# Kernel optimization log

Measured on AMD Instinct MI355X. Metric: run time of the kernel, lower is better.

## Reference

```python
import jax, jax.numpy as jnp
import numpy as np

FIRST_USER_FEATURE = 64
TOP_K = 10
SIG_TAU = 1.0
TAU_NDCG = 0.1
TAU_DIV = 0.1
EPS = 1e-10
SINKHORN_ITERS = 5


def sinkhorn_scaling(mat):
    # Fixed 5 iterations (torch version has a data-dependent early break with
    # tol=1e-6 that essentially never triggers at these temperatures).
    for _ in range(SINKHORN_ITERS):
        mat = mat / jnp.clip(mat.sum(axis=1, keepdims=True), EPS)
        mat = mat / jnp.clip(mat.sum(axis=2, keepdims=True), EPS)
    return mat


def calc_p_sort(score, tau):
    # NeuralSort-style soft permutation. score: (U, N) -> p: (U, N, N)
    s = score.astype(jnp.float32)
    N = s.shape[-1]
    # A_k = sum_j |s_k - s_j|  (matches a_s.sum(dim=-1) in torch; symmetric)
    a_sum = jnp.abs(s[:, :, None] - s[:, None, :]).sum(axis=-1)  # (U, N)
    v = (N + 1 - 2 * jnp.arange(1, N + 1)).astype(jnp.float32)   # (N,)
    logits = v[None, :, None] * s[:, None, :] - a_sum[:, None, :]  # (U, N, N)
    p = jax.nn.softmax(logits / tau, axis=-1)
    return sinkhorn_scaling(p)


def calc_dcg(rel):
    # rel: (U, N); take first TOP_K positions, log2 discount
    r = rel[:, :TOP_K]
    disc = jnp.log2(jnp.arange(2, TOP_K + 2, dtype=jnp.float32))
    return ((2.0 ** r - 1.0) / disc).sum(axis=1)


def calc_ndcg(p_sort, score, rel):
    approx_rel = jnp.einsum('uij,uj->ui', p_sort, rel.astype(jnp.float32))
    approx_dcg = calc_dcg(approx_rel)
    idx = jnp.argsort(-score, axis=1)  # descending sort indices
    rel_by_model = jnp.take_along_axis(rel, idx, axis=1)
    dcg = calc_dcg(rel_by_model)
    best_dcg = calc_dcg(-jnp.sort(-rel, axis=1))
    return approx_dcg / best_dcg, dcg / best_dcg


def dissimilarity_metric(items):
    # 1 - pairwise cosine similarity between item feature vectors. items: (U,N,F)
    n = items / jnp.clip(jnp.linalg.norm(items, axis=-1, keepdims=True), 1e-8)
    return 1.0 - jnp.einsum('uif,ujf->uij', n, n)


def calc_diversity(batch, score, p_sort):
    items = batch[:, :, :FIRST_USER_FEATURE]
    N = batch.shape[1]
    w = jnp.arange(N, 0, -1, dtype=jnp.float32)                  # row weights N..1
    approx_rank = jnp.einsum('uij,i->uj', p_sort, w)             # (U, N)
    approx_rank = jax.nn.sigmoid(SIG_TAU * (approx_rank - (N - TOP_K)))
    # zero_below_diagonal == keep strictly-upper triangle
    approx_mat = jnp.triu(approx_rank[:, :, None] * approx_rank[:, None, :], k=1)
    # real rank: rank 1 = lowest score, rank N = highest (argsort of argsort)
    real_rank = (jnp.argsort(jnp.argsort(score, axis=1), axis=1) + 1).astype(jnp.float32)
    real_rank = jnp.clip(real_rank - (N - TOP_K), 0.0, 1.0)
    real_mat = jnp.triu(real_rank[:, :, None] * real_rank[:, None, :], k=1)
    dis = jnp.triu(dissimilarity_metric(items), k=1)
    approx_div = (approx_mat * dis).sum(axis=(1, 2)) / jax.lax.stop_gradient(approx_mat.sum(axis=(1, 2)))
    div = (real_mat * dis).sum(axis=(1, 2)) / real_mat.sum(axis=(1, 2))
    return approx_div, div


def setup_inputs() -> dict:
    key = jax.random.key(0)
    k1, k2, k3, k4 = jax.random.split(key, 4)
    U, N, F = 128, 512, 80
    return {
        'batch': jax.random.normal(k1, (U, N, F), dtype=jnp.float32),
        'model_score_for_div': jax.random.normal(k2, (U, N), dtype=jnp.float32),
        'model_score_for_ndcg': jax.random.normal(k3, (U, N), dtype=jnp.float32),
        'relevance': jax.random.uniform(k4, (U, N), dtype=jnp.float32),
    }


def reference(batch, model_score_for_div, model_score_for_ndcg, relevance):
    p_ndcg = calc_p_sort(model_score_for_ndcg, TAU_NDCG)
    approx_ndcg, ndcg_score = calc_ndcg(p_ndcg, model_score_for_ndcg, relevance)
    p_div = calc_p_sort(model_score_for_div, TAU_DIV)
    approx_div, div_score = calc_diversity(batch, model_score_for_div, p_div)
    return approx_ndcg, ndcg_score, approx_div, div_score
```

## Files before the change

kernel.cpp:

```cpp
#include <hip/hip_runtime.h>

#define N 512
#define U_CNT 128
#define F_STRIDE 80
#define TOPK 10
#define W 32
#define PAD 64
#define BSZ (PAD + N + PAD)
#define NCH ((2 * W + 4) / 4)
#define BAND (2 * W + 4)
#define L2T 14.426950408889634f
#define LOG2E 1.4426950408889634f
#define NEGBIG -1.0e30f

#if defined(__has_builtin)
#if __has_builtin(__builtin_amdgcn_exp2f)
#define EXP2F(x) __builtin_amdgcn_exp2f(x)
#endif
#if __has_builtin(__builtin_amdgcn_logf)
#define LOG2F(x) __builtin_amdgcn_logf(x)
#endif
#endif
#ifndef EXP2F
#define EXP2F(x) exp2f(x)
#endif
#ifndef LOG2F
#define LOG2F(x) log2f(x)
#endif

__device__ __forceinline__ unsigned long long sortkey(float x, int idx) {
  unsigned int bb = __float_as_uint(x);
  bb ^= (unsigned int)((int)bb >> 31) | 0x80000000u;
  return ((unsigned long long)(~bb) << 10) | (unsigned long long)idx;
}

__global__ __launch_bounds__(512, 2) void loss_kernel(
    const float* __restrict__ batch, const float* __restrict__ sdiv,
    const float* __restrict__ sndcg, const float* __restrict__ rel,
    float* __restrict__ out) {
  __shared__ __align__(16) unsigned long long bkA[N];
  __shared__ __align__(16) unsigned long long bkB[N];
  __shared__ __align__(16) int sh_hist[2][256];
  __shared__ __align__(16) int sh_cur[2][256];
  __shared__ __align__(16) int sh_offs[2][257];
  __shared__ int sh_wt[8];
  __shared__ __align__(16) float sh_sv[N];
  __shared__ __align__(16) int sh_pos[N];
  __shared__ __align__(16) float sh_Qs[BSZ];
  __shared__ __align__(16) float sh_Uu[BSZ];
  __shared__ __align__(16) float sh_Rl[BSZ];
  __shared__ __align__(16) float sh_r[BSZ];
  __shared__ __align__(16) float sh_c[BSZ];
  __shared__ __align__(16) float sh_lw[BSZ];
  __shared__ __align__(16) float sh_relS[N];
  __shared__ __align__(16) float sh_aux[N];
  __shared__ __align__(16) float sh_inv[N];
  __shared__ __align__(16) float sh_rr[N];
  __shared__ __align__(16) float sh_pA[N];
  __shared__ __align__(16) float sh_pB[N];
  __shared__ float sh_red[8];
  __shared__ float sh_w1[8], sh_w2[8], sh_w3[8], sh_w4[8], sh_w5[8];
  __shared__ float sh_row[TOPK];
  __shared__ float sh_invd[16];

  const int b = blockIdx.x;
  const int u = b >> 1;
  const int which = b & 1;
  const int t = threadIdx.x;
  const int wv = t >> 6;
  const int ln = t & 63;

  if (t < PAD) {
    sh_Qs[t] = 0.f; sh_Uu[t] = NEGBIG; sh_Rl[t] = NEGBIG;
    sh_r[t] = 0.f; sh_c[t] = 0.f;
    sh_lw[t] = which ? 0.f : NEGBIG;
    if (t < 16) sh_invd[t] = 1.f / LOG2F((float)(t + 2));
  } else if (t < 2 * PAD) {
    int p = N + t;
    sh_Qs[p] = 0.f; sh_Uu[p] = NEGBIG; sh_Rl[p] = NEGBIG;
    sh_r[p] = 0.f; sh_c[p] = 0.f;
    sh_lw[p] = which ? 0.f : NEGBIG;
  }
  {
    int half = t >> 8, tt = t & 255;
    sh_hist[half][tt] = 0;
    sh_cur[half][tt] = 0;
  }

  const float sj = ((which ? sdiv : sndcg) + (size_t)u * N)[t];
  const unsigned long long myk = sortkey(sj, t);
  int bA = (int)fmaf(sj, 32.f, 128.f);
  bA = min(max(bA, 0), 255);
  float rv = 0.f;
  unsigned long long myk2 = 0;
  int bB = 0;
  if (!which) {
    rv = rel[(size_t)u * N + t];
    myk2 = sortkey(rv, t);
    bB = min(max((int)(rv * 256.f), 0), 255);
  }
  float ssq = 0.f;
  if (which) {
    const float4* it4 =
        (const float4*)(batch + (size_t)(u * N + t) * F_STRIDE);
#pragma unroll
    for (int f4 = 0; f4 < 16; f4++) {
      float4 p = it4[f4];
      ssq = fmaf(p.x, p.x, ssq); ssq = fmaf(p.y, p.y, ssq);
      ssq = fmaf(p.z, p.z, ssq); ssq = fmaf(p.w, p.w, ssq);
    }
  }
  __syncthreads();

  atomicAdd(&sh_hist[0][bA], 1);
  if (!which) atomicAdd(&sh_hist[1][bB], 1);
  __syncthreads();

  {
    int half = t >> 8, tt = t & 255;
    int h = 0, ps = 0;
    bool act = (half == 0) || (!which);
    if (act) {
      h = sh_hist[half][tt];
      ps = h;
#pragma unroll
      for (int m = 1; m <= 32; m <<= 1) {
        int o = __shfl_up(ps, m, 64);
        if (ln >= m) ps += o;
      }
      if (ln == 63) sh_wt[(tt >> 6) | (half << 2)] = ps;
    }
    __syncthreads();
    if (act) {
      int w0 = (tt >> 6) | (half << 2);
      int off = 0;
#pragma unroll
      for (int w2 = 0; w2 < 4; w2++) {
        int wi = (half << 2) + w2;
        if (wi < w0) off += sh_wt[wi];
      }
      int ex = ps - h + off;
      sh_offs[half][tt] = ex;
      if (tt == 255) sh_offs[half][256] = ex + h;
    }
  }
  __syncthreads();

  {
    int sA = sh_offs[0][bA] + atomicAdd(&sh_cur[0][bA], 1);
    bkA[sA] = myk;
    if (!which) {
      int sB = sh_offs[1][bB] + atomicAdd(&sh_cur[1][bB], 1);
      bkB[sB] = myk2;
    }
  }
  __syncthreads();

  int rnk2 = 0;
  {
    int lo = sh_offs[0][bA], hi = sh_offs[0][bA + 1];
    int rnk = N - hi;
    for (int k = lo; k < hi; k++) rnk += (bkA[k] < myk);
    sh_sv[rnk] = sj;
    sh_pos[rnk] = t;
    if (!which) {
      sh_relS[rnk] = rv;
      int lo2 = sh_offs[1][bB], hi2 = sh_offs[1][bB + 1];
      rnk2 = N - hi2;
      for (int k = lo2; k < hi2; k++) rnk2 += (bkB[k] < myk2);
    }
  }
  __syncthreads();

  const float sv = sh_sv[t];
  sh_Qs[PAD + t] = sv * L2T;
  {
    float ps = sv;
#pragma unroll
    for (int m = 1; m <= 32; m <<= 1) {
      float o = __shfl_up(ps, m, 64);
      if (ln >= m) ps += o;
    }
    if (ln == 63) sh_red[wv] = ps;
    __syncthreads();
    float off = 0.f, Tt = 0.f;
#pragma unroll
    for (int w2 = 0; w2 < 8; w2++) {
      float rw = sh_red[w2];
      if (w2 < wv) off += rw;
      Tt += rw;
    }
    float S = ps + off;
    float asum = 2.f * S - Tt + (float)(N - 2 - 2 * t) * sv;
    sh_Uu[PAD + t] = -asum * L2T;
  }
  __syncthreads();

  const int base = (t & ~3) - W;
  const float vi = 511.f - 2.f * (float)t;

  float4 Krow[NCH], Kcol[NCH];
  float rt = 1.f, ct;

  {
    float e0 = fmaf(vi, sh_Qs[PAD + t - 1], sh_Uu[PAD + t - 1]);
    float e1 = fmaf(vi, sh_Qs[PAD + t], sh_Uu[PAD + t]);
    float e2 = fmaf(vi, sh_Qs[PAD + t + 1], sh_Uu[PAD + t + 1]);
    float em = -fmaxf(e1, fmaxf(e0, e2));
    const float4* q4 = (const float4*)(sh_Qs + PAD + base);
    const float4* u4 = (const float4*)(sh_Uu + PAD + base);
    float z0 = 0.f, z1 = 0.f, z2 = 0.f, z3 = 0.f;
#pragma unroll
    for (int c = 0; c < NCH; c++) {
      float4 a = q4[c], cc = u4[c];
      float t0 = EXP2F(fmaf(vi, a.x, cc.x) + em);
      float t1 = EXP2F(fmaf(vi, a.y, cc.y) + em);
      float t2 = EXP2F(fmaf(vi, a.z, cc.z) + em);
      float t3 = EXP2F(fmaf(vi, a.w, cc.w) + em);
      Krow[c].x = t0; Krow[c].y = t1; Krow[c].z = t2; Krow[c].w = t3;
      z0 += t0; z1 += t1; z2 += t2; z3 += t3;
    }
    float Z = (z0 + z2) + (z1 + z3);
    float invZ = 1.f / Z;
    sh_Rl[PAD + t] = em - LOG2F(Z);
#pragma unroll
    for (int c = 0; c < NCH; c++) {
      Krow[c].x *= invZ; Krow[c].y *= invZ;
      Krow[c].z *= invZ; Krow[c].w *= invZ;
    }
  }
  __syncthreads();

  {
    const float qsr = sh_Qs[PAD + t];
    const float c0 = sh_Uu[PAD + t];
    const float4* r4 = (const float4*)(sh_Rl + PAD + base);
    float a0 = 0.f, a1 = 0.f, a2 = 0.f, a3 = 0.f;
    float v = 511.f - 2.f * (float)base;
#pragma unroll
    for (int c = 0; c < NCH; c++) {
      float4 r = r4[c];
      float t0 = EXP2F(fmaf(v, qsr, c0) + r.x); v -= 2.f;
      float t1 = EXP2F(fmaf(v, qsr, c0) + r.y); v -= 2.f;
      float t2 = EXP2F(fmaf(v, qsr, c0) + r.z); v -= 2.f;
      float t3 = EXP2F(fmaf(v, qsr, c0) + r.w); v -= 2.f;
      Kcol[c].x = t0; Kcol[c].y = t1; Kcol[c].z = t2; Kcol[c].w = t3;
      a0 += t0; a1 += t1; a2 += t2; a3 += t3;
    }
    float A = (a0 + a2) + (a1 + a3);
    ct = 1.f / fmaxf(A, 1e-10f);
    sh_c[PAD + t] = ct;
  }
  __syncthreads();

#pragma unroll 1
  for (int it = 0; it < 5; it++) {
    {
      const float4* c4 = (const float4*)(sh_c + PAD + base);
      float a0 = 0.f, a1 = 0.f, a2 = 0.f, a3 = 0.f;
#pragma unroll
      for (int c = 0; c < NCH; c++) {
        float4 cc = c4[c];
        a0 = fmaf(Krow[c].x, cc.x, a0);
        a1 = fmaf(Krow[c].y, cc.y, a1);
        a2 = fmaf(Krow[c].z, cc.z, a2);
        a3 = fmaf(Krow[c].w, cc.w, a3);
      }
      float A = (a0 + a2) + (a1 + a3);
      float trues = rt * A;
      rt = rt / fmaxf(trues, 1e-10f);
      sh_r[PAD + t] = rt;
      if (it == 4) {
        if (which)
          sh_lw[PAD + t] = (float)(N - t) * rt;
        else
          sh_lw[PAD + t] = sh_Uu[PAD + t] + LOG2F(ct);
      }
    }
    __syncthreads();
    if (it < 4) {
      {
        const float4* r4 = (const float4*)(sh_r + PAD + base);
        float a0 = 0.f, a1 = 0.f, a2 = 0.f, a3 = 0.f;
#pragma unroll
        for (int c = 0; c < NCH; c++) {
          float4 rr = r4[c];
          a0 = fmaf(Kcol[c].x, rr.x, a0);
          a1 = fmaf(Kcol[c].y, rr.y, a1);
          a2 = fmaf(Kcol[c].z, rr.z, a2);
          a3 = fmaf(Kcol[c].w, rr.w, a3);
        }
        float A = (a0 + a2) + (a1 + a3);
        float trues = ct * A;
        ct = ct / fmaxf(trues, 1e-10f);
        sh_c[PAD + t] = ct;
      }
      __syncthreads();
    }
  }

  if (which == 0) {
#pragma unroll
    for (int r = wv; r < TOPK; r += 8) {
      const float cv = 511.f - 2.f * (float)r;
      const float rl = sh_Rl[PAD + r];
      const float rr = sh_r[PAD + r];
      const int rbase = (r & ~3) - W;
      float srel = 0.f;
#pragma unroll
      for (int k = 0; k < 2; k++) {
        int e = ln + 64 * k;
        if (e < BAND) {
          int j = rbase + e;
          float ex = fmaf(cv, sh_Qs[PAD + j], sh_lw[PAD + j]) + rl;
          float rv2 = ((unsigned)j < N) ? sh_relS[j] : 0.f;
          srel = fmaf(EXP2F(ex), rv2, srel);
        }
      }
#pragma unroll
      for (int mm = 32; mm >= 1; mm >>= 1) srel += __shfl_xor(srel, mm, 64);
      if (ln == 0) sh_row[r] = srel * rr;
    }
    float cd = (t < TOPK) ? (EXP2F(sh_relS[t]) - 1.f) * sh_invd[t] : 0.f;
    float cb = 0.f;
    if (rnk2 < TOPK) cb = (EXP2F(rv) - 1.f) * sh_invd[rnk2];
#pragma unroll
    for (int mm = 32; mm >= 1; mm >>= 1) {
      cd += __shfl_xor(cd, mm, 64);
      cb += __shfl_xor(cb, mm, 64);
    }
    if (ln == 0) { sh_w1[wv] = cd; sh_w2[wv] = cb; }
    __syncthreads();
    if (t == 0) {
      float adcg = 0.f;
#pragma unroll
      for (int r = 0; r < TOPK; r++)
        adcg += (EXP2F(sh_row[r]) - 1.f) * sh_invd[r];
      float dcg = 0.f, bdcg = 0.f;
#pragma unroll
      for (int w2 = 0; w2 < 8; w2++) { dcg += sh_w1[w2]; bdcg += sh_w2[w2]; }
      out[u] = adcg / bdcg;
      out[U_CNT + u] = dcg / bdcg;
    }
  } else {
    {
      const float4* l4 = (const float4*)(sh_lw + PAD + base);
      float a0 = 0.f, a1 = 0.f, a2 = 0.f, a3 = 0.f;
#pragma unroll
      for (int c = 0; c < NCH; c++) {
        float4 r = l4[c];
        a0 = fmaf(Kcol[c].x, r.x, a0);
        a1 = fmaf(Kcol[c].y, r.y, a1);
        a2 = fmaf(Kcol[c].z, r.z, a2);
        a3 = fmaf(Kcol[c].w, r.w, a3);
      }
      float ar = ct * ((a0 + a2) + (a1 + a3));
      float arj_s = 1.f / (1.f + EXP2F((502.f - ar) * LOG2E));
      int o = sh_pos[t];
      sh_aux[o] = arj_s;
      sh_rr[o] = (t < TOPK) ? 1.f : 0.f;
    }
    float inv = 1.f / fmaxf(sqrtf(ssq), 1e-8f);
    sh_inv[t] = inv;
    float om = 1.f - ssq * inv * inv;
    __syncthreads();
    float arj = sh_aux[t], rrj = sh_rr[t];
    float r1 = arj, r2 = arj * arj, r3 = arj * arj * om, r4v = rrj,
          r5v = rrj * om;
#pragma unroll
    for (int mm = 32; mm >= 1; mm >>= 1) {
      r1 += __shfl_xor(r1, mm, 64);
      r2 += __shfl_xor(r2, mm, 64);
      r3 += __shfl_xor(r3, mm, 64);
      r4v += __shfl_xor(r4v, mm, 64);
      r5v += __shfl_xor(r5v, mm, 64);
    }
    if (ln == 0) {
      sh_w1[wv] = r1; sh_w2[wv] = r2; sh_w3[wv] = r3;
      sh_w4[wv] = r4v; sh_w5[wv] = r5v;
    }
    const float* bu = batch + (size_t)u * N * F_STRIDE;
    float va = 0.f, vr = 0.f;
#pragma unroll 8
    for (int jj = 0; jj < 64; jj++) {
      int j2 = (wv << 6) + jj;
      float x = bu[(size_t)j2 * F_STRIDE + ln] * sh_inv[j2];
      va = fmaf(sh_aux[j2], x, va);
      vr = fmaf(sh_rr[j2], x, vr);
    }
    sh_pA[t] = va;
    sh_pB[t] = vr;
    __syncthreads();
    float qa = 0.f, qr = 0.f;
    if (t < 64) {
      float VA = 0.f, VR = 0.f;
#pragma unroll
      for (int c2 = 0; c2 < 8; c2++) {
        VA += sh_pA[c2 * 64 + t];
        VR += sh_pB[c2 * 64 + t];
      }
      qa = VA * VA;
      qr = VR * VR;
    }
#pragma unroll
    for (int mm = 32; mm >= 1; mm >>= 1) {
      qa += __shfl_xor(qa, mm, 64);
      qr += __shfl_xor(qr, mm, 64);
    }
    if (t == 0) {
      float S1a = 0.f, S2a = 0.f, DA = 0.f, S1r = 0.f, DR = 0.f;
#pragma unroll
      for (int w2 = 0; w2 < 8; w2++) {
        S1a += sh_w1[w2]; S2a += sh_w2[w2]; DA += sh_w3[w2];
        S1r += sh_w4[w2]; DR += sh_w5[w2];
      }
      float numA = 0.5f * (S1a * S1a - qa - DA);
      float denA = 0.5f * (S1a * S1a - S2a);
      out[2 * U_CNT + u] = numA / denA;
      float numR = 0.5f * (S1r * S1r - qr - DR);
      float denR = 0.5f * (S1r * S1r - S1r);
      out[3 * U_CNT + u] = numR / denR;
    }
  }
}

extern "C" void kernel_launch(void* const* d_in, const int* in_sizes, int n_in,
                              void* d_out, int out_size, void* d_ws,
                              size_t ws_size, hipStream_t stream) {
  (void)in_sizes; (void)n_in; (void)d_ws; (void)ws_size; (void)out_size;
  const float* batch = (const float*)d_in[0];
  const float* sdiv = (const float*)d_in[1];
  const float* sndcg = (const float*)d_in[2];
  const float* rel = (const float*)d_in[3];
  float* out = (float*)d_out;
  loss_kernel<<<dim3(U_CNT * 2), dim3(N), 0, stream>>>(batch, sdiv, sndcg, rel,
                                                       out);
}
```

Baseline: 24.24 us.

## Narrow softmax band width and compute histogram prefix sum in a single wave

Shrinks the banded window half-width W from 32 to 24, so the band (2W+4=52) fits in one 64-lane pass and the second loop iteration is removed. Separately, it replaces the two-stage block-wide histogram scan (with its shared partial-sum array and extra barrier) with a single wave per half that loads four bins per lane as int4 and does one shuffle scan. The narrower band drops soft-permutation mass farther from the diagonal, which risks accuracy at this temperature, and the one-wave scan serializes work that was spread over more waves.

```diff
diff --git a/kernel.cpp b/kernel.cpp
--- a/kernel.cpp
+++ b/kernel.cpp
@@ -4,7 +4,7 @@
 #define U_CNT 128
 #define F_STRIDE 80
 #define TOPK 10
-#define W 32
+#define W 24
 #define PAD 64
 #define BSZ (PAD + N + PAD)
 #define NCH ((2 * W + 4) / 4)
@@ -42,8 +42,7 @@
   __shared__ __align__(16) unsigned long long bkB[N];
   __shared__ __align__(16) int sh_hist[2][256];
   __shared__ __align__(16) int sh_cur[2][256];
-  __shared__ __align__(16) int sh_offs[2][257];
-  __shared__ int sh_wt[8];
+  __shared__ __align__(16) int sh_offs[2][260];
   __shared__ __align__(16) float sh_sv[N];
   __shared__ __align__(16) int sh_pos[N];
   __shared__ __align__(16) float sh_Qs[BSZ];
@@ -116,33 +115,21 @@
   if (!which) atomicAdd(&sh_hist[1][bB], 1);
   __syncthreads();
 
-  {
-    int half = t >> 8, tt = t & 255;
-    int h = 0, ps = 0;
-    bool act = (half == 0) || (!which);
-    if (act) {
-      h = sh_hist[half][tt];
-      ps = h;
-#pragma unroll
-      for (int m = 1; m <= 32; m <<= 1) {
-        int o = __shfl_up(ps, m, 64);
-        if (ln >= m) ps += o;
-      }
-      if (ln == 63) sh_wt[(tt >> 6) | (half << 2)] = ps;
-    }
-    __syncthreads();
-    if (act) {
-      int w0 = (tt >> 6) | (half << 2);
-      int off = 0;
-#pragma unroll
-      for (int w2 = 0; w2 < 4; w2++) {
-        int wi = (half << 2) + w2;
-        if (wi < w0) off += sh_wt[wi];
-      }
-      int ex = ps - h + off;
-      sh_offs[half][tt] = ex;
-      if (tt == 255) sh_offs[half][256] = ex + h;
-    }
+  if (wv == 0 || (wv == 4 && !which)) {
+    int half = wv >> 2;
+    int4 h = ((const int4*)sh_hist[half])[ln];
+    int hs = h.x + h.y + h.z + h.w;
+    int ps = hs;
+#pragma unroll
+    for (int m = 1; m <= 32; m <<= 1) {
+      int o = __shfl_up(ps, m, 64);
+      if (ln >= m) ps += o;
+    }
+    int e0 = ps - hs;
+    int4 e;
+    e.x = e0; e.y = e0 + h.x; e.z = e.y + h.y; e.w = e.z + h.z;
+    ((int4*)sh_offs[half])[ln] = e;
+    if (ln == 63) sh_offs[half][256] = ps;
   }
   __syncthreads();
 
@@ -307,9 +294,8 @@
       const float rr = sh_r[PAD + r];
       const int rbase = (r & ~3) - W;
       float srel = 0.f;
-#pragma unroll
-      for (int k = 0; k < 2; k++) {
-        int e = ln + 64 * k;
+      {
+        int e = ln;
         if (e < BAND) {
           int j = rbase + e;
           float ex = fmaf(cv, sh_Qs[PAD + j], sh_lw[PAD + j]) + rl;
```

Result: faster. 21.78 us (-10.1%).
